# Kernel optimization log

Measured on AMD Instinct MI355X. Metric: run time of the kernel, lower is better.

## Reference

```python
import jax, jax.numpy as jnp
import numpy as np


def _dsc(x, dw, db, pw, pb):
    # depthwise 3x3 (groups = in_channels) then pointwise 1x1, both with bias
    c = x.shape[1]
    y = jax.lax.conv_general_dilated(
        x, dw, window_strides=(1, 1), padding='SAME',
        dimension_numbers=('NCHW', 'OIHW', 'NCHW'), feature_group_count=c)
    y = y + db[None, :, None, None]
    y = jnp.einsum('bchw,oc->bohw', y, pw) + pb[None, :, None, None]
    return y


def _chan_attn(q, k, v):
    # channel attention with softmax over the FLATTENED c*c matrix (not per-row).
    # NOTE: original uses k.view(b, w*h, c) which is a reshape, NOT a transpose.
    b, c, w, h = q.shape
    wh = w * h
    qk = jnp.matmul(q.reshape(b, c, wh), k.reshape(b, wh, c)) / jnp.sqrt(jnp.float32(wh))
    qk = jax.nn.softmax(qk.reshape(b, c * c), axis=1).reshape(b, c, c)
    return jnp.matmul(qk, v.reshape(b, c, wh)).reshape(b, c, w, h)


def setup_inputs() -> dict:
    key = jax.random.key(0)
    ks = jax.random.split(key, 16)
    b, c, w, h = 8, 64, 256, 256
    s = 0.05
    d = {
        'x': jax.random.normal(ks[0], (b, c, w, h), jnp.float32),
        'mask': jax.random.normal(ks[1], (b, c, w, h), jnp.float32),
        'avg_ct': jax.random.normal(ks[2], (b, c, w, h), jnp.float32),
    }
    for i, p in enumerate(['q', 'k', 'v']):
        d[f'dw_{p}'] = jax.random.normal(ks[3 + 4 * i], (c, 1, 3, 3), jnp.float32) * s
        d[f'db_{p}'] = jax.random.normal(ks[4 + 4 * i], (c,), jnp.float32) * s
        d[f'pw_{p}'] = jax.random.normal(ks[5 + 4 * i], (c, c), jnp.float32) * s
        d[f'pb_{p}'] = jax.random.normal(ks[6 + 4 * i], (c,), jnp.float32) * s
    return d


def reference(x, mask, avg_ct,
              dw_q, db_q, pw_q, pb_q,
              dw_k, db_k, pw_k, pb_k,
              dw_v, db_v, pw_v, pb_v):
    # shared projections (q1==q2, k1..k4 identical, v1==v3, q3==q4, v2==v4)
    q_x = _dsc(x, dw_q, db_q, pw_q, pb_q)
    k_x = _dsc(x, dw_k, db_k, pw_k, pb_k)
    v_x = _dsc(x, dw_v, db_v, pw_v, pb_v)
    q_m = _dsc(mask, dw_q, db_q, pw_q, pb_q)
    v_a = _dsc(avg_ct, dw_v, db_v, pw_v, pb_v)

    sa = _chan_attn(q_x, k_x, v_x)
    ma_wo_mask = _chan_attn(q_x, k_x, v_a)
    ma_wo_avgct = _chan_attn(q_m, k_x, v_x)
    ha = _chan_attn(q_m, k_x, v_a)
    return sa + ma_wo_avgct + ma_wo_mask + ha + x
```

## Files before the change

### kernel.cpp

```cpp
#include <hip/hip_runtime.h>
#include <hip/hip_bf16.h>
#include <stdint.h>

#define DI __device__ __forceinline__

typedef unsigned short u16;
typedef unsigned int   u32;

DI float bf2f(u32 v){ u32 x = v << 16; float f; __builtin_memcpy(&f, &x, 4); return f; }
DI u16 f2bf(float f){ u32 x; __builtin_memcpy(&x, &f, 4); u32 r = (x + 0x7fffu + ((x >> 16) & 1u)) >> 16; return (u16)r; }

DI void unpack8(uint4 v, float* f){
  f[0]=bf2f(v.x & 0xffffu); f[1]=bf2f(v.x >> 16);
  f[2]=bf2f(v.y & 0xffffu); f[3]=bf2f(v.y >> 16);
  f[4]=bf2f(v.z & 0xffffu); f[5]=bf2f(v.z >> 16);
  f[6]=bf2f(v.w & 0xffffu); f[7]=bf2f(v.w >> 16);
}

DI void load_row18(const float* p, bool rowv, bool leftv, bool rightv, float* r){
  if(rowv){
    const float4* p4 = (const float4*)p;
    #pragma unroll
    for(int q=0;q<4;q++){ float4 v = p4[q]; r[1+4*q]=v.x; r[2+4*q]=v.y; r[3+4*q]=v.z; r[4+4*q]=v.w; }
    r[0]  = leftv  ? p[-1] : 0.f;
    r[17] = rightv ? p[16] : 0.f;
  } else {
    #pragma unroll
    for(int q=0;q<18;q++) r[q]=0.f;
  }
}
DI void load_row18_add(const float* p, bool rowv, bool leftv, bool rightv, float* r){
  if(rowv){
    const float4* p4 = (const float4*)p;
    #pragma unroll
    for(int q=0;q<4;q++){ float4 v = p4[q]; r[1+4*q]+=v.x; r[2+4*q]+=v.y; r[3+4*q]+=v.z; r[4+4*q]+=v.w; }
    if(leftv)  r[0]  += p[-1];
    if(rightv) r[17] += p[16];
  }
}
DI void conv16(const float r[3][18], const float* w, float* y){
  #pragma unroll
  for(int p=0;p<16;p++){
    float s =      r[0][p]   * w[0];
    s = fmaf(r[0][p+1], w[1], s);
    s = fmaf(r[0][p+2], w[2], s);
    s = fmaf(r[1][p],   w[3], s);
    s = fmaf(r[1][p+1], w[4], s);
    s = fmaf(r[1][p+2], w[5], s);
    s = fmaf(r[2][p],   w[6], s);
    s = fmaf(r[2][p+1], w[7], s);
    s = fmaf(r[2][p+2], w[8], s);
    y[p] = s;
  }
}
DI void store16bf(u16* p, const float* y, float add){
  #pragma unroll
  for(int h=0;h<2;h++){
    union { u16 s[8]; uint4 v; } pk;
    #pragma unroll
    for(int q=0;q<8;q++) pk.s[q] = f2bf(y[h*8+q] + add);
    ((uint4*)p)[h] = pk.v;
  }
}

__global__ __launch_bounds__(256) void k1_dsc(
    const float* __restrict__ x, const float* __restrict__ mask_, const float* __restrict__ avg,
    const float* __restrict__ dwq, const float* __restrict__ dbq,
    const float* __restrict__ dwk, const float* __restrict__ dbk,
    const float* __restrict__ pwk, const float* __restrict__ pbk,
    const float* __restrict__ dwv, const float* __restrict__ dbv,
    u16* __restrict__ Dqx, u16* __restrict__ Dqm, u16* __restrict__ Kx, u16* __restrict__ Dvs)
{
  __shared__ __align__(16) float dwkL[64*68];
  __shared__ __align__(16) float pwTL[64*68];
  int t = threadIdx.x;
  int bid = blockIdx.x;
  int tile = bid & 3, iw = (bid>>2)&255, b = bid>>10;

  for(int idx=t; idx<4096; idx+=256)
    pwTL[(idx&63)*68 + (idx>>6)] = pwk[idx];

  int ch = t>>2, pg = t&3;
  int ih0 = tile*64 + pg*16;
  bool leftv = ih0 > 0, rightv = ih0 < 240;
  long base = ((long)(b*64+ch)<<16) + (iw<<8) + ih0;
  bool r0v = iw > 0, r2v = iw < 255;

  float rx[3][18];
  load_row18(x + base - 256, r0v, leftv, rightv, rx[0]);
  load_row18(x + base,       true, leftv, rightv, rx[1]);
  load_row18(x + base + 256, r2v, leftv, rightv, rx[2]);
  float y[16];
  { float w[9];
    #pragma unroll
    for(int q=0;q<9;q++) w[q]=dwq[ch*9+q];
    conv16(rx, w, y); store16bf(Dqx + base, y, dbq[ch]); }
  { float w[9];
    #pragma unroll
    for(int q=0;q<9;q++) w[q]=dwk[ch*9+q];
    conv16(rx, w, y);
    float bk = dbk[ch];
    #pragma unroll
    for(int p=0;p<16;p++) dwkL[ch*68 + pg*16 + p] = y[p] + bk; }
  load_row18_add(avg + base - 256, r0v, leftv, rightv, rx[0]);
  load_row18_add(avg + base,       true, leftv, rightv, rx[1]);
  load_row18_add(avg + base + 256, r2v, leftv, rightv, rx[2]);
  { float w[9];
    #pragma unroll
    for(int q=0;q<9;q++) w[q]=dwv[ch*9+q];
    conv16(rx, w, y); store16bf(Dvs + base, y, 2.f*dbv[ch]); }
  load_row18(mask_ + base - 256, r0v, leftv, rightv, rx[0]);
  load_row18(mask_ + base,       true, leftv, rightv, rx[1]);
  load_row18(mask_ + base + 256, r2v, leftv, rightv, rx[2]);
  { float w[9];
    #pragma unroll
    for(int q=0;q<9;q++) w[q]=dwq[ch*9+q];
    conv16(rx, w, y); store16bf(Dqm + base, y, dbq[ch]); }

  __syncthreads();
  int o0 = (t>>4)*4, px0 = (t&15)*4;
  float acc[4][4];
  #pragma unroll
  for(int oo=0;oo<4;oo++){ float pb = pbk[o0+oo];
    #pragma unroll
    for(int pp=0;pp<4;pp++) acc[oo][pp]=pb; }
  for(int a=0;a<64;a++){
    float4 pv4 = *(const float4*)(pwTL + a*68 + o0);
    float4 dv4 = *(const float4*)(dwkL + a*68 + px0);
    float pv[4]={pv4.x,pv4.y,pv4.z,pv4.w};
    float dv[4]={dv4.x,dv4.y,dv4.z,dv4.w};
    #pragma unroll
    for(int oo=0;oo<4;oo++)
      #pragma unroll
      for(int pp=0;pp<4;pp++) acc[oo][pp] = fmaf(pv[oo], dv[pp], acc[oo][pp]);
  }
  #pragma unroll
  for(int oo=0;oo<4;oo++){
    union{ u16 s[4]; uint2 v; } pk;
    #pragma unroll
    for(int pp=0;pp<4;pp++) pk.s[pp] = f2bf(acc[oo][pp]);
    long kb = ((long)(b*64+o0+oo)<<16) + (iw<<8) + tile*64 + px0;
    *(uint2*)(Kx + kb) = pk.v;
  }
}

__global__ __launch_bounds__(256) void k2_qk(
    const u16* __restrict__ Dqx, const u16* __restrict__ Dqm, const u16* __restrict__ Kx,
    float* __restrict__ part, float* __restrict__ part_r)
{
  __shared__ __align__(16) float q1L[64*68];
  __shared__ __align__(16) float q2L[64*68];
  __shared__ __align__(16) float kcL[64*68];
  __shared__ float rbuf[4*64];
  int t = threadIdx.x;
  int pb = blockIdx.x;
  int uh = pb & 1, ch = (pb>>1)&63, b = pb>>7;
  int li = t>>2, lu0 = (t&3)*16;
  long qoff = ((long)(b*64+li)<<16) + (ch<<10) + uh*512;
  long koff = ((long)(b*64+ch)<<16) + (long)(uh*512)*64;
  float acc1[4][4] = {{0}}; float acc2[4][4] = {{0}};
  float rs[16];
  #pragma unroll
  for(int m=0;m<16;m++) rs[m]=0.f;

  for(int c0=0;c0<8;c0++){
    int u0 = c0*64;
    if(c0) __syncthreads();
    { const uint4* p = (const uint4*)(Dqx + qoff + u0 + lu0);
      float f[16]; unpack8(p[0], f); unpack8(p[1], f+8);
      #pragma unroll
      for(int m=0;m<16;m++) q1L[(lu0+m)*68 + li] = f[m]; }
    { const uint4* p = (const uint4*)(Dqm + qoff + u0 + lu0);
      float f[16]; unpack8(p[0], f); unpack8(p[1], f+8);
      #pragma unroll
      for(int m=0;m<16;m++) q2L[(lu0+m)*68 + li] = f[m]; }
    { const uint4* p = (const uint4*)(Kx + koff + (long)((u0 + li)*64 + lu0));
      float f[16]; unpack8(p[0], f); unpack8(p[1], f+8);
      float* dst = kcL + li*68 + lu0;
      *(float4*)(dst)    = make_float4(f[0],f[1],f[2],f[3]);
      *(float4*)(dst+4)  = make_float4(f[4],f[5],f[6],f[7]);
      *(float4*)(dst+8)  = make_float4(f[8],f[9],f[10],f[11]);
      *(float4*)(dst+12) = make_float4(f[12],f[13],f[14],f[15]);
      #pragma unroll
      for(int m=0;m<16;m++) rs[m] += f[m]; }
    __syncthreads();
    int i0 = (t>>4)*4, j0 = (t&15)*4;
    #pragma unroll 8
    for(int uu=0; uu<64; uu++){
      float4 kv4 = *(const float4*)(kcL + uu*68 + j0);
      float4 q14 = *(const float4*)(q1L + uu*68 + i0);
      float4 q24 = *(const float4*)(q2L + uu*68 + i0);
      float kv[4]={kv4.x,kv4.y,kv4.z,kv4.w};
      float q1[4]={q14.x,q14.y,q14.z,q14.w};
      float q2[4]={q24.x,q24.y,q24.z,q24.w};
      #pragma unroll
      for(int ii=0;ii<4;ii++)
        #pragma unroll
        for(int jj=0;jj<4;jj++){
          acc1[ii][jj] = fmaf(q1[ii], kv[jj], acc1[ii][jj]);
          acc2[ii][jj] = fmaf(q2[ii], kv[jj], acc2[ii][jj]);
        }
    }
  }
  { int i0 = (t>>4)*4, j0 = (t&15)*4;
    float* p1 = part + ((long)pb*2)*4096;
    float* p2 = p1 + 4096;
    #pragma unroll
    for(int ii=0;ii<4;ii++){
      *(float4*)(p1 + (i0+ii)*64 + j0) = make_float4(acc1[ii][0],acc1[ii][1],acc1[ii][2],acc1[ii][3]);
      *(float4*)(p2 + (i0+ii)*64 + j0) = make_float4(acc2[ii][0],acc2[ii][1],acc2[ii][2],acc2[ii][3]);
    } }
  #pragma unroll
  for(int off=4; off<64; off<<=1)
    #pragma unroll
    for(int m=0;m<16;m++) rs[m] += __shfl_xor(rs[m], off);
  if((t&63) < 4){
    int wv = t>>6, jg = t&3;
    #pragma unroll
    for(int m=0;m<16;m++) rbuf[wv*64 + jg*16 + m] = rs[m];
  }
  __syncthreads();
  if(t < 64)
    part_r[(long)pb*64 + t] = rbuf[t] + rbuf[64+t] + rbuf[128+t] + rbuf[192+t];
}

__global__ __launch_bounds__(256) void k2b_reduce(
    const float* __restrict__ part, const float* __restrict__ part_r,
    float* __restrict__ M1, float* __restrict__ M2, float* __restrict__ rsum)
{
  int t = threadIdx.x;
  int blk = blockIdx.x;
  if(blk < 256){
    int e = blk*256 + t;
    int mat = e >> 15;
    int b = (e >> 12) & 7;
    int ij = e & 4095;
    float s = 0.f;
    const float* p = part + ((long)b*256 + mat)*4096 + ij;
    for(int cu=0; cu<128; cu++) s += p[(long)cu*8192];
    (mat ? M2 : M1)[b*4096 + ij] = s;
  } else {
    for(int e=t; e<512; e+=256){
      int bb = e>>6, j = e&63;
      float s=0.f;
      const float* p = part_r + (long)bb*8192 + j;
      for(int cu=0;cu<128;cu++) s += p[cu*64];
      rsum[bb*64 + j] = s;
    }
  }
}

__global__ __launch_bounds__(256) void k3_small(
    const float* __restrict__ M1, const float* __restrict__ M2, const float* __restrict__ rsum,
    const float* __restrict__ pwq, const float* __restrict__ pbq,
    const float* __restrict__ pwv, const float* __restrict__ pbv,
    float* __restrict__ Tt, float* __restrict__ cvec)
{
  __shared__ __align__(16) float ML[64*68];
  __shared__ __align__(16) float SL[64*68];
  __shared__ float red[8];
  __shared__ float rL[64];
  int b = blockIdx.x, t = threadIdx.x;
  if(t < 64) rL[t] = rsum[b*64 + t];
  int i = t>>2, j0 = (t&3)*16;
  float pq = pbq[i];
  for(int m=0; m<2; m++){
    const float* M = (m ? M2 : M1) + b*4096;
    __syncthreads();
    for(int idx=t; idx<4096; idx+=256)
      ML[(idx>>6)*68 + (idx&63)] = M[idx];
    __syncthreads();
    float l[16];
    #pragma unroll
    for(int q=0;q<16;q++) l[q] = pq * rL[j0+q];
    for(int a=0;a<64;a++){
      float w = pwq[i*64 + a];
      #pragma unroll
      for(int q=0;q<16;q++) l[q] = fmaf(w, ML[a*68 + j0 + q], l[q]);
    }
    float mx = -1e30f;
    #pragma unroll
    for(int q=0;q<16;q++){ l[q] *= 0.00390625f; mx = fmaxf(mx, l[q]); }
    for(int off=1; off<64; off<<=1) mx = fmaxf(mx, __shfl_xor(mx, off));
    if((t&63)==0) red[t>>6] = mx;
    __syncthreads();
    mx = fmaxf(fmaxf(red[0],red[1]), fmaxf(red[2],red[3]));
    float e[16]; float s = 0.f;
    #pragma unroll
    for(int q=0;q<16;q++){ e[q] = __expf(l[q]-mx); s += e[q]; }
    for(int off=1; off<64; off<<=1) s += __shfl_xor(s, off);
    if((t&63)==0) red[4 + (t>>6)] = s;
    __syncthreads();
    float inv = 1.f / (red[4]+red[5]+red[6]+red[7]);
    if(m==0){
      #pragma unroll
      for(int q=0;q<16;q++) SL[i*68 + j0 + q] = e[q]*inv;
    } else {
      #pragma unroll
      for(int q=0;q<16;q++) SL[i*68 + j0 + q] += e[q]*inv;
    }
  }
  __syncthreads();
  int a0 = (t&3)*16;
  float tacc[16];
  #pragma unroll
  for(int q=0;q<16;q++) tacc[q]=0.f;
  float cv = 0.f;
  for(int j=0;j<64;j++){
    float sij = SL[i*68 + j];
    const float* pr = pwv + j*64 + a0;
    #pragma unroll
    for(int q=0;q<16;q++) tacc[q] = fmaf(sij, pr[q], tacc[q]);
    cv = fmaf(sij, pbv[j], cv);
  }
  #pragma unroll
  for(int q=0;q<16;q++) Tt[b*4096 + (a0+q)*64 + i] = tacc[q];
  if((t&3)==0) cvec[b*64 + i] = 2.f*cv;
}

__global__ __launch_bounds__(256) void k4_out(
    const u16* __restrict__ Dvs, const float* __restrict__ Tt, const float* __restrict__ cvec,
    const float* __restrict__ x, float* __restrict__ out)
{
  __shared__ __align__(16) float TT[64*68];
  __shared__ __align__(16) float DL[64*68];
  __shared__ float cvL[64];
  int t = threadIdx.x;
  int bid = blockIdx.x;
  int tile = bid & 3, iw = (bid>>2)&255, b = bid>>10;
  int s0 = (iw<<8) + tile*64;
  if(t < 64) cvL[t] = cvec[b*64 + t];
  { int a = t>>2, ii0 = (t&3)*16;
    const float4* p = (const float4*)(Tt + b*4096 + a*64 + ii0);
    float4* d = (float4*)(TT + a*68 + ii0);
    d[0]=p[0]; d[1]=p[1]; d[2]=p[2]; d[3]=p[3]; }
  { int a = t>>2, pp0 = (t&3)*16;
    const uint4* p = (const uint4*)(Dvs + ((long)(b*64+a)<<16) + s0 + pp0);
    float f[16]; unpack8(p[0], f); unpack8(p[1], f+8);
    float* d = DL + a*68 + pp0;
    *(float4*)(d)    = make_float4(f[0],f[1],f[2],f[3]);
    *(float4*)(d+4)  = make_float4(f[4],f[5],f[6],f[7]);
    *(float4*)(d+8)  = make_float4(f[8],f[9],f[10],f[11]);
    *(float4*)(d+12) = make_float4(f[12],f[13],f[14],f[15]); }
  __syncthreads();
  int i0 = (t>>4)*4, p0 = (t&15)*4;
  float acc[4][4] = {{0}};
  for(int a=0;a<64;a++){
    float4 tv4 = *(const float4*)(TT + a*68 + i0);
    float4 dv4 = *(const float4*)(DL + a*68 + p0);
    float tv[4]={tv4.x,tv4.y,tv4.z,tv4.w};
    float dv[4]={dv4.x,dv4.y,dv4.z,dv4.w};
    #pragma unroll
    for(int ii=0;ii<4;ii++)
      #pragma unroll
      for(int pp=0;pp<4;pp++) acc[ii][pp] = fmaf(tv[ii], dv[pp], acc[ii][pp]);
  }
  #pragma unroll
  for(int ii=0;ii<4;ii++){
    int row = i0+ii;
    long g = ((long)(b*64+row)<<16) + s0 + p0;
    float4 xv = *(const float4*)(x + g);
    float cv = cvL[row];
    float4 o;
    o.x = acc[ii][0] + cv + xv.x;
    o.y = acc[ii][1] + cv + xv.y;
    o.z = acc[ii][2] + cv + xv.z;
    o.w = acc[ii][3] + cv + xv.w;
    *(float4*)(out + g) = o;
  }
}

extern "C" void kernel_launch(void* const* d_in, const int* in_sizes, int n_in,
                              void* d_out, int out_size, void* d_ws, size_t ws_size,
                              hipStream_t stream)
{
  const float* x    = (const float*)d_in[0];
  const float* mask = (const float*)d_in[1];
  const float* avg  = (const float*)d_in[2];
  const float* dwq  = (const float*)d_in[3];
  const float* dbq  = (const float*)d_in[4];
  const float* pwq  = (const float*)d_in[5];
  const float* pbq  = (const float*)d_in[6];
  const float* dwk  = (const float*)d_in[7];
  const float* dbk  = (const float*)d_in[8];
  const float* pwk  = (const float*)d_in[9];
  const float* pbk  = (const float*)d_in[10];
  const float* dwv  = (const float*)d_in[11];
  const float* dbv  = (const float*)d_in[12];
  const float* pwv  = (const float*)d_in[13];
  const float* pbv  = (const float*)d_in[14];
  float* out = (float*)d_out;
  char* ws = (char*)d_ws;

  u16* Dqx     = (u16*)(ws);
  u16* Dqm     = (u16*)(ws + 67108864);
  u16* Kx      = (u16*)(ws + 134217728);
  u16* Dvs     = (u16*)(ws + 201326592);
  float* part   = (float*)(ws + 268435456);
  float* part_r = (float*)(ws + 301989888);
  float* M1     = (float*)(ws + 302252032);
  float* M2     = (float*)(ws + 302383104);
  float* rsum   = (float*)(ws + 302514176);
  float* Tt     = (float*)(ws + 302516224);
  float* cvec   = (float*)(ws + 302647296);

  hipLaunchKernelGGL(k1_dsc, dim3(8192), dim3(256), 0, stream,
      x, mask, avg, dwq, dbq, dwk, dbk, pwk, pbk, dwv, dbv, Dqx, Dqm, Kx, Dvs);
  hipLaunchKernelGGL(k2_qk, dim3(1024), dim3(256), 0, stream, Dqx, Dqm, Kx, part, part_r);
  hipLaunchKernelGGL(k2b_reduce, dim3(257), dim3(256), 0, stream, part, part_r, M1, M2, rsum);
  hipLaunchKernelGGL(k3_small, dim3(8), dim3(256), 0, stream, M1, M2, rsum, pwq, pbq, pwv, pbv, Tt, cvec);
  hipLaunchKernelGGL(k4_out, dim3(8192), dim3(256), 0, stream, Dvs, Tt, cvec, x, out);
}
```

Measured before the change: 844.5 us.

## Use bf16 MFMA for QK partials and output matmul with transposed V layout

Replaces the scalar FMA loops in the QK partial kernel and the output kernel with 16x16x32 bf16 MFMA instructions. The depthwise V result is now written channel-contiguous (transposed through shared memory in the first kernel), and the T matrix is stored as bf16 so both MFMA operands can be loaded directly. The aim is to cut ALU time and shared-memory staging in the two matmul kernels. In exchange it adds an extra LDS transpose pass in k1, stores T in bf16 instead of fp32, and makes k4 write the output one scalar per lane with a 16-element stride, which may hurt store coalescing.

```diff
diff --git a/kernel.cpp b/kernel.cpp
--- a/kernel.cpp
+++ b/kernel.cpp
@@ -6,16 +6,11 @@
 
 typedef unsigned short u16;
 typedef unsigned int   u32;
+typedef __attribute__((ext_vector_type(8))) short short8;
+typedef __attribute__((ext_vector_type(4))) float f32x4;
 
 DI float bf2f(u32 v){ u32 x = v << 16; float f; __builtin_memcpy(&f, &x, 4); return f; }
 DI u16 f2bf(float f){ u32 x; __builtin_memcpy(&x, &f, 4); u32 r = (x + 0x7fffu + ((x >> 16) & 1u)) >> 16; return (u16)r; }
-
-DI void unpack8(uint4 v, float* f){
-  f[0]=bf2f(v.x & 0xffffu); f[1]=bf2f(v.x >> 16);
-  f[2]=bf2f(v.y & 0xffffu); f[3]=bf2f(v.y >> 16);
-  f[4]=bf2f(v.z & 0xffffu); f[5]=bf2f(v.z >> 16);
-  f[6]=bf2f(v.w & 0xffffu); f[7]=bf2f(v.w >> 16);
-}
 
 DI void load_row18(const float* p, bool rowv, bool leftv, bool rightv, float* r){
   if(rowv){
@@ -69,7 +64,7 @@
     const float* __restrict__ dwk, const float* __restrict__ dbk,
     const float* __restrict__ pwk, const float* __restrict__ pbk,
     const float* __restrict__ dwv, const float* __restrict__ dbv,
-    u16* __restrict__ Dqx, u16* __restrict__ Dqm, u16* __restrict__ Kx, u16* __restrict__ Dvs)
+    u16* __restrict__ Dqx, u16* __restrict__ Dqm, u16* __restrict__ Kx, u16* __restrict__ DvsT)
 {
   __shared__ __align__(16) float dwkL[64*68];
   __shared__ __align__(16) float pwTL[64*68];
@@ -102,13 +97,17 @@
     float bk = dbk[ch];
     #pragma unroll
     for(int p=0;p<16;p++) dwkL[ch*68 + pg*16 + p] = y[p] + bk; }
+  float yv[16];
   load_row18_add(avg + base - 256, r0v, leftv, rightv, rx[0]);
   load_row18_add(avg + base,       true, leftv, rightv, rx[1]);
   load_row18_add(avg + base + 256, r2v, leftv, rightv, rx[2]);
   { float w[9];
     #pragma unroll
     for(int q=0;q<9;q++) w[q]=dwv[ch*9+q];
-    conv16(rx, w, y); store16bf(Dvs + base, y, 2.f*dbv[ch]); }
+    conv16(rx, w, yv);
+    float bv = 2.f*dbv[ch];
+    #pragma unroll
+    for(int p=0;p<16;p++) yv[p] += bv; }
   load_row18(mask_ + base - 256, r0v, leftv, rightv, rx[0]);
   load_row18(mask_ + base,       true, leftv, rightv, rx[1]);
   load_row18(mask_ + base + 256, r2v, leftv, rightv, rx[2]);
@@ -142,86 +141,104 @@
     long kb = ((long)(b*64+o0+oo)<<16) + (iw<<8) + tile*64 + px0;
     *(uint2*)(Kx + kb) = pk.v;
   }
+
+  __syncthreads();
+  float* dvsL = dwkL;
+  #pragma unroll
+  for(int p=0;p<16;p++) dvsL[(pg*16+p)*68 + ch] = yv[p];
+  __syncthreads();
+  { int sl = t>>2, c0 = (t&3)*16;
+    const float4* rp = (const float4*)(dvsL + sl*68 + c0);
+    float4 v0=rp[0], v1=rp[1], v2=rp[2], v3=rp[3];
+    float f[16] = {v0.x,v0.y,v0.z,v0.w, v1.x,v1.y,v1.z,v1.w,
+                   v2.x,v2.y,v2.z,v2.w, v3.x,v3.y,v3.z,v3.w};
+    union{ u16 s[8]; uint4 v; } pa, pb2;
+    #pragma unroll
+    for(int q=0;q<8;q++){ pa.s[q]=f2bf(f[q]); pb2.s[q]=f2bf(f[8+q]); }
+    long db = ((long)b<<22) + (long)((iw<<8) + tile*64 + sl)*64 + c0;
+    ((uint4*)(DvsT + db))[0] = pa.v;
+    ((uint4*)(DvsT + db))[1] = pb2.v;
+  }
 }
 
 __global__ __launch_bounds__(256) void k2_qk(
     const u16* __restrict__ Dqx, const u16* __restrict__ Dqm, const u16* __restrict__ Kx,
     float* __restrict__ part, float* __restrict__ part_r)
 {
-  __shared__ __align__(16) float q1L[64*68];
-  __shared__ __align__(16) float q2L[64*68];
-  __shared__ __align__(16) float kcL[64*68];
-  __shared__ float rbuf[4*64];
+  __shared__ u32 bt[64*33];
   int t = threadIdx.x;
   int pb = blockIdx.x;
   int uh = pb & 1, ch = (pb>>1)&63, b = pb>>7;
-  int li = t>>2, lu0 = (t&3)*16;
-  long qoff = ((long)(b*64+li)<<16) + (ch<<10) + uh*512;
-  long koff = ((long)(b*64+ch)<<16) + (long)(uh*512)*64;
-  float acc1[4][4] = {{0}}; float acc2[4][4] = {{0}};
-  float rs[16];
-  #pragma unroll
-  for(int m=0;m<16;m++) rs[m]=0.f;
-
-  for(int c0=0;c0<8;c0++){
-    int u0 = c0*64;
-    if(c0) __syncthreads();
-    { const uint4* p = (const uint4*)(Dqx + qoff + u0 + lu0);
-      float f[16]; unpack8(p[0], f); unpack8(p[1], f+8);
-      #pragma unroll
-      for(int m=0;m<16;m++) q1L[(lu0+m)*68 + li] = f[m]; }
-    { const uint4* p = (const uint4*)(Dqm + qoff + u0 + lu0);
-      float f[16]; unpack8(p[0], f); unpack8(p[1], f+8);
-      #pragma unroll
-      for(int m=0;m<16;m++) q2L[(lu0+m)*68 + li] = f[m]; }
-    { const uint4* p = (const uint4*)(Kx + koff + (long)((u0 + li)*64 + lu0));
-      float f[16]; unpack8(p[0], f); unpack8(p[1], f+8);
-      float* dst = kcL + li*68 + lu0;
-      *(float4*)(dst)    = make_float4(f[0],f[1],f[2],f[3]);
-      *(float4*)(dst+4)  = make_float4(f[4],f[5],f[6],f[7]);
-      *(float4*)(dst+8)  = make_float4(f[8],f[9],f[10],f[11]);
-      *(float4*)(dst+12) = make_float4(f[12],f[13],f[14],f[15]);
-      #pragma unroll
-      for(int m=0;m<16;m++) rs[m] += f[m]; }
+  int w = t>>6, lane = t&63;
+  int quad = lane>>4, n = lane&15;
+
+  f32x4 z = {0.f,0.f,0.f,0.f};
+  f32x4 acc1[4] = {z,z,z,z};
+  f32x4 acc2[4] = {z,z,z,z};
+  float rs[4] = {0.f,0.f,0.f,0.f};
+
+  long aoff = ((long)(b*64 + w*16 + n)<<16) + ch*1024 + uh*512 + quad*8;
+  const u16* A1 = Dqx + aoff;
+  const u16* A2 = Dqm + aoff;
+  const u16* Bg = Kx + ((long)(b*64+ch)<<16) + (long)(uh*512)*64;
+  int r2 = t>>3, c0s = (t&7)*8;
+
+  for(int cu=0; cu<8; cu++){
+    const u16* src = Bg + cu*4096;
+    uint4 ra = *(const uint4*)(src + (2*r2)*64 + c0s);
+    uint4 rb = *(const uint4*)(src + (2*r2+1)*64 + c0s);
+    if(cu) __syncthreads();
+    { u32 aw[4] = {ra.x,ra.y,ra.z,ra.w};
+      u32 bw[4] = {rb.x,rb.y,rb.z,rb.w};
+      #pragma unroll
+      for(int k=0;k<4;k++){
+        u32 lo = (aw[k]&0xffffu) | (bw[k]<<16);
+        u32 hi = (aw[k]>>16) | (bw[k]&0xffff0000u);
+        int c = c0s + 2*k;
+        bt[c*33 + r2]     = lo;
+        bt[(c+1)*33 + r2] = hi;
+      } }
     __syncthreads();
-    int i0 = (t>>4)*4, j0 = (t&15)*4;
-    #pragma unroll 8
-    for(int uu=0; uu<64; uu++){
-      float4 kv4 = *(const float4*)(kcL + uu*68 + j0);
-      float4 q14 = *(const float4*)(q1L + uu*68 + i0);
-      float4 q24 = *(const float4*)(q2L + uu*68 + i0);
-      float kv[4]={kv4.x,kv4.y,kv4.z,kv4.w};
-      float q1[4]={q14.x,q14.y,q14.z,q14.w};
-      float q2[4]={q24.x,q24.y,q24.z,q24.w};
-      #pragma unroll
-      for(int ii=0;ii<4;ii++)
+    #pragma unroll
+    for(int ks=0; ks<2; ks++){
+      int koff = cu*64 + ks*32;
+      short8 a1 = *(const short8*)(A1 + koff);
+      short8 a2 = *(const short8*)(A2 + koff);
+      #pragma unroll
+      for(int c=0;c<4;c++){
+        union{ u32 wv[4]; short8 v; } bf;
         #pragma unroll
-        for(int jj=0;jj<4;jj++){
-          acc1[ii][jj] = fmaf(q1[ii], kv[jj], acc1[ii][jj]);
-          acc2[ii][jj] = fmaf(q2[ii], kv[jj], acc2[ii][jj]);
+        for(int i=0;i<4;i++) bf.wv[i] = bt[(c*16+n)*33 + ks*16 + quad*4 + i];
+        acc1[c] = __builtin_amdgcn_mfma_f32_16x16x32_bf16(a1, bf.v, acc1[c], 0,0,0);
+        acc2[c] = __builtin_amdgcn_mfma_f32_16x16x32_bf16(a2, bf.v, acc2[c], 0,0,0);
+        if(w==0){
+          #pragma unroll
+          for(int i=0;i<4;i++) rs[c] += bf2f(bf.wv[i]&0xffffu) + bf2f(bf.wv[i]>>16);
         }
-    }
-  }
-  { int i0 = (t>>4)*4, j0 = (t&15)*4;
-    float* p1 = part + ((long)pb*2)*4096;
-    float* p2 = p1 + 4096;
-    #pragma unroll
-    for(int ii=0;ii<4;ii++){
-      *(float4*)(p1 + (i0+ii)*64 + j0) = make_float4(acc1[ii][0],acc1[ii][1],acc1[ii][2],acc1[ii][3]);
-      *(float4*)(p2 + (i0+ii)*64 + j0) = make_float4(acc2[ii][0],acc2[ii][1],acc2[ii][2],acc2[ii][3]);
-    } }
-  #pragma unroll
-  for(int off=4; off<64; off<<=1)
-    #pragma unroll
-    for(int m=0;m<16;m++) rs[m] += __shfl_xor(rs[m], off);
-  if((t&63) < 4){
-    int wv = t>>6, jg = t&3;
-    #pragma unroll
-    for(int m=0;m<16;m++) rbuf[wv*64 + jg*16 + m] = rs[m];
-  }
-  __syncthreads();
-  if(t < 64)
-    part_r[(long)pb*64 + t] = rbuf[t] + rbuf[64+t] + rbuf[128+t] + rbuf[192+t];
+      }
+    }
+  }
+  float* p1 = part + (long)pb*8192;
+  float* p2 = p1 + 4096;
+  #pragma unroll
+  for(int c=0;c<4;c++)
+    #pragma unroll
+    for(int r=0;r<4;r++){
+      int ar = w*16 + quad*4 + r;
+      p1[ar*64 + c*16 + n] = acc1[c][r];
+      p2[ar*64 + c*16 + n] = acc2[c][r];
+    }
+  if(w==0){
+    #pragma unroll
+    for(int c=0;c<4;c++){
+      rs[c] += __shfl_xor(rs[c], 16);
+      rs[c] += __shfl_xor(rs[c], 32);
+    }
+    if(lane < 16){
+      #pragma unroll
+      for(int c=0;c<4;c++) part_r[(long)pb*64 + c*16 + lane] = rs[c];
+    }
+  }
 }
 
 __global__ __launch_bounds__(256) void k2b_reduce(
@@ -254,7 +271,7 @@
     const float* __restrict__ M1, const float* __restrict__ M2, const float* __restrict__ rsum,
     const float* __restrict__ pwq, const float* __restrict__ pbq,
     const float* __restrict__ pwv, const float* __restrict__ pbv,
-    float* __restrict__ Tt, float* __restrict__ cvec)
+    u16* __restrict__ Tb, float* __restrict__ cvec)
 {
   __shared__ __align__(16) float ML[64*68];
   __shared__ __align__(16) float SL[64*68];
@@ -313,60 +330,46 @@
     for(int q=0;q<16;q++) tacc[q] = fmaf(sij, pr[q], tacc[q]);
     cv = fmaf(sij, pbv[j], cv);
   }
-  #pragma unroll
-  for(int q=0;q<16;q++) Tt[b*4096 + (a0+q)*64 + i] = tacc[q];
+  { union{ u16 s[8]; uint4 v; } pa, pb2;
+    #pragma unroll
+    for(int q=0;q<8;q++){ pa.s[q]=f2bf(tacc[q]); pb2.s[q]=f2bf(tacc[8+q]); }
+    ((uint4*)(Tb + b*4096 + i*64 + a0))[0] = pa.v;
+    ((uint4*)(Tb + b*4096 + i*64 + a0))[1] = pb2.v;
+  }
   if((t&3)==0) cvec[b*64 + i] = 2.f*cv;
 }
 
 __global__ __launch_bounds__(256) void k4_out(
-    const u16* __restrict__ Dvs, const float* __restrict__ Tt, const float* __restrict__ cvec,
+    const u16* __restrict__ DvsT, const u16* __restrict__ Tb, const float* __restrict__ cvec,
     const float* __restrict__ x, float* __restrict__ out)
 {
-  __shared__ __align__(16) float TT[64*68];
-  __shared__ __align__(16) float DL[64*68];
   __shared__ float cvL[64];
   int t = threadIdx.x;
   int bid = blockIdx.x;
-  int tile = bid & 3, iw = (bid>>2)&255, b = bid>>10;
-  int s0 = (iw<<8) + tile*64;
+  int sc = bid & 511, b = bid >> 9;
+  int s0 = sc * 128;
   if(t < 64) cvL[t] = cvec[b*64 + t];
-  { int a = t>>2, ii0 = (t&3)*16;
-    const float4* p = (const float4*)(Tt + b*4096 + a*64 + ii0);
-    float4* d = (float4*)(TT + a*68 + ii0);
-    d[0]=p[0]; d[1]=p[1]; d[2]=p[2]; d[3]=p[3]; }
-  { int a = t>>2, pp0 = (t&3)*16;
-    const uint4* p = (const uint4*)(Dvs + ((long)(b*64+a)<<16) + s0 + pp0);
-    float f[16]; unpack8(p[0], f); unpack8(p[1], f+8);
-    float* d = DL + a*68 + pp0;
-    *(float4*)(d)    = make_float4(f[0],f[1],f[2],f[3]);
-    *(float4*)(d+4)  = make_float4(f[4],f[5],f[6],f[7]);
-    *(float4*)(d+8)  = make_float4(f[8],f[9],f[10],f[11]);
-    *(float4*)(d+12) = make_float4(f[12],f[13],f[14],f[15]); }
   __syncthreads();
-  int i0 = (t>>4)*4, p0 = (t&15)*4;
-  float acc[4][4] = {{0}};
-  for(int a=0;a<64;a++){
-    float4 tv4 = *(const float4*)(TT + a*68 + i0);
-    float4 dv4 = *(const float4*)(DL + a*68 + p0);
-    float tv[4]={tv4.x,tv4.y,tv4.z,tv4.w};
-    float dv[4]={dv4.x,dv4.y,dv4.z,dv4.w};
-    #pragma unroll
-    for(int ii=0;ii<4;ii++)
-      #pragma unroll
-      for(int pp=0;pp<4;pp++) acc[ii][pp] = fmaf(tv[ii], dv[pp], acc[ii][pp]);
-  }
-  #pragma unroll
-  for(int ii=0;ii<4;ii++){
-    int row = i0+ii;
-    long g = ((long)(b*64+row)<<16) + s0 + p0;
-    float4 xv = *(const float4*)(x + g);
-    float cv = cvL[row];
-    float4 o;
-    o.x = acc[ii][0] + cv + xv.x;
-    o.y = acc[ii][1] + cv + xv.y;
-    o.z = acc[ii][2] + cv + xv.z;
-    o.w = acc[ii][3] + cv + xv.w;
-    *(float4*)(out + g) = o;
+  int w = t>>6, lane = t&63;
+  int quad = lane>>4, n = lane&15;
+  const u16* Ap = Tb + b*4096 + (w*16 + n)*64 + quad*8;
+  short8 a0 = *(const short8*)(Ap);
+  short8 a1 = *(const short8*)(Ap + 32);
+  const u16* Bp = DvsT + ((long)b<<22) + (long)(s0 + n)*64 + quad*8;
+  #pragma unroll
+  for(int c=0;c<8;c++){
+    short8 b0 = *(const short8*)(Bp + c*1024);
+    short8 b1 = *(const short8*)(Bp + c*1024 + 32);
+    f32x4 acc = {0.f,0.f,0.f,0.f};
+    acc = __builtin_amdgcn_mfma_f32_16x16x32_bf16(a0, b0, acc, 0,0,0);
+    acc = __builtin_amdgcn_mfma_f32_16x16x32_bf16(a1, b1, acc, 0,0,0);
+    int scol = s0 + c*16 + n;
+    #pragma unroll
+    for(int r=0;r<4;r++){
+      int i = w*16 + quad*4 + r;
+      long g = ((long)(b*64+i)<<16) + scol;
+      out[g] = acc[r] + cvL[i] + x[g];
+    }
   }
 }
 
@@ -392,22 +395,22 @@
   float* out = (float*)d_out;
   char* ws = (char*)d_ws;
 
-  u16* Dqx     = (u16*)(ws);
-  u16* Dqm     = (u16*)(ws + 67108864);
-  u16* Kx      = (u16*)(ws + 134217728);
-  u16* Dvs     = (u16*)(ws + 201326592);
+  u16* Dqx      = (u16*)(ws);
+  u16* Dqm      = (u16*)(ws + 67108864);
+  u16* Kx       = (u16*)(ws + 134217728);
+  u16* DvsT     = (u16*)(ws + 201326592);
   float* part   = (float*)(ws + 268435456);
   float* part_r = (float*)(ws + 301989888);
   float* M1     = (float*)(ws + 302252032);
   float* M2     = (float*)(ws + 302383104);
   float* rsum   = (float*)(ws + 302514176);
-  float* Tt     = (float*)(ws + 302516224);
-  float* cvec   = (float*)(ws + 302647296);
+  u16*   Tb     = (u16*)(ws + 302516224);
+  float* cvec   = (float*)(ws + 302581760);
 
   hipLaunchKernelGGL(k1_dsc, dim3(8192), dim3(256), 0, stream,
-      x, mask, avg, dwq, dbq, dwk, dbk, pwk, pbk, dwv, dbv, Dqx, Dqm, Kx, Dvs);
+      x, mask, avg, dwq, dbq, dwk, dbk, pwk, pbk, dwv, dbv, Dqx, Dqm, Kx, DvsT);
   hipLaunchKernelGGL(k2_qk, dim3(1024), dim3(256), 0, stream, Dqx, Dqm, Kx, part, part_r);
   hipLaunchKernelGGL(k2b_reduce, dim3(257), dim3(256), 0, stream, part, part_r, M1, M2, rsum);
-  hipLaunchKernelGGL(k3_small, dim3(8), dim3(256), 0, stream, M1, M2, rsum, pwq, pbq, pwv, pbv, Tt, cvec);
-  hipLaunchKernelGGL(k4_out, dim3(8192), dim3(256), 0, stream, Dvs, Tt, cvec, x, out);
-}
+  hipLaunchKernelGGL(k3_small, dim3(8), dim3(256), 0, stream, M1, M2, rsum, pwq, pbq, pwv, pbv, Tb, cvec);
+  hipLaunchKernelGGL(k4_out, dim3(4096), dim3(256), 0, stream, DvsT, Tb, cvec, x, out);
+}
```

Measured after the change: 817.3 us. 3.2% less time.
